# Kernel optimization log

Measured on AMD Instinct MI355X. Metric: run time of the kernel, lower is better.

## Reference

```python
import jax, jax.numpy as jnp
import numpy as np

NUM_FEAS = 4096
HID = 128
BATCH = 128


def setup_inputs() -> dict:
    key = jax.random.key(0)
    k1, k2, k3, k4 = jax.random.split(key, 4)
    batch_x = jax.random.normal(k1, (BATCH, NUM_FEAS), dtype=jnp.float32)
    C = jax.random.normal(k2, (1, HID), dtype=jnp.float32)
    W = jax.random.normal(k3, (NUM_FEAS, HID), dtype=jnp.float32)
    B = jax.random.normal(k4, (NUM_FEAS,), dtype=jnp.float32)
    return {"batch_x": batch_x, "C": C, "W": W, "B": B}


def reference(batch_x, C, W, B):
    # binarize input (matches (x > 0).float())
    x = (batch_x > 0).astype(jnp.float32)  # [B, F]
    # prefix sums: S_excl[b, i] = sum_{j < i} x[b, j] * W[j]   -> [B, F, H]
    contrib = x[:, :, None] * W[None, :, :]
    S = jnp.cumsum(contrib, axis=1)
    S_excl = jnp.concatenate([jnp.zeros_like(S[:, :1]), S[:, :-1]], axis=1)
    # hidden state for i >= 1: h_i = sigmoid(S_excl_i + C)
    h = jax.nn.sigmoid(S_excl + C[None, :, :])  # [B, F, H]
    # faithful quirk: for i == 0 the original uses raw C (no sigmoid)
    h = h.at[:, 0, :].set(jnp.broadcast_to(C[0], (x.shape[0], HID)))
    # logits z_i = h_i . W_i + B_i ; p_i = sigmoid(z_i)
    z = jnp.einsum('bfh,fh->bf', h, W) + B[None, :]
    # BCE(sum over features), stable via log_sigmoid
    log_p = jax.nn.log_sigmoid(z)
    log_q = jax.nn.log_sigmoid(-z)
    loss_per_sample = -jnp.sum(x * log_p + (1.0 - x) * log_q, axis=1)
    return jnp.mean(loss_per_sample)
```

## Files before the change

### kernel.cpp

```cpp
#include <hip/hip_runtime.h>

#define NFEAS 4096
#define HID   128
#define BATCH 128
#define NSUB  64
#define NCH   16
#define KF    256
#define L2E   1.4426950408889634f
#define LN2   0.6931471805599453f

__device__ __forceinline__ float scan64(float v) {
  float r = v; int y;
  y = __builtin_amdgcn_update_dpp(0, __float_as_int(r), 0x111, 0xF, 0xF, true); r += __int_as_float(y);
  y = __builtin_amdgcn_update_dpp(0, __float_as_int(r), 0x112, 0xF, 0xF, true); r += __int_as_float(y);
  y = __builtin_amdgcn_update_dpp(0, __float_as_int(r), 0x114, 0xF, 0xF, true); r += __int_as_float(y);
  y = __builtin_amdgcn_update_dpp(0, __float_as_int(r), 0x118, 0xF, 0xF, true); r += __int_as_float(y);
  y = __builtin_amdgcn_update_dpp(0, __float_as_int(r), 0x142, 0xA, 0xF, true); r += __int_as_float(y);
  y = __builtin_amdgcn_update_dpp(0, __float_as_int(r), 0x143, 0xC, 0xF, true); r += __int_as_float(y);
  return r;
}

__device__ __forceinline__ void scan64_x8(float& a, float& b, float& c, float& d,
                                          float& e, float& f, float& g, float& h) {
  int t0, t1, t2, t3, t4, t5, t6, t7;
#define S8(ctrl, rm)                                                              \
  t0 = __builtin_amdgcn_update_dpp(0, __float_as_int(a), ctrl, rm, 0xF, true);    \
  t1 = __builtin_amdgcn_update_dpp(0, __float_as_int(b), ctrl, rm, 0xF, true);    \
  t2 = __builtin_amdgcn_update_dpp(0, __float_as_int(c), ctrl, rm, 0xF, true);    \
  t3 = __builtin_amdgcn_update_dpp(0, __float_as_int(d), ctrl, rm, 0xF, true);    \
  t4 = __builtin_amdgcn_update_dpp(0, __float_as_int(e), ctrl, rm, 0xF, true);    \
  t5 = __builtin_amdgcn_update_dpp(0, __float_as_int(f), ctrl, rm, 0xF, true);    \
  t6 = __builtin_amdgcn_update_dpp(0, __float_as_int(g), ctrl, rm, 0xF, true);    \
  t7 = __builtin_amdgcn_update_dpp(0, __float_as_int(h), ctrl, rm, 0xF, true);    \
  a += __int_as_float(t0); b += __int_as_float(t1);                               \
  c += __int_as_float(t2); d += __int_as_float(t3);                               \
  e += __int_as_float(t4); f += __int_as_float(t5);                               \
  g += __int_as_float(t6); h += __int_as_float(t7);
  S8(0x111, 0xF) S8(0x112, 0xF) S8(0x114, 0xF) S8(0x118, 0xF)
  S8(0x142, 0xA) S8(0x143, 0xC)
#undef S8
}

__global__ __launch_bounds__(128) void chunk_sums_kernel(
    const float* __restrict__ x, const float* __restrict__ W,
    float* __restrict__ T)
{
  __shared__ float xm[64][8];
  const int c = blockIdx.x, g = blockIdx.y, t = threadIdx.x;

  {
    const int s = t >> 4, fb = (t & 15) << 2;
    const float4 v = *reinterpret_cast<const float4*>(
        &x[(size_t)(g * 8 + s) * NFEAS + c * 64 + fb]);
    xm[fb + 0][s] = v.x > 0.f ? 1.f : 0.f;
    xm[fb + 1][s] = v.y > 0.f ? 1.f : 0.f;
    xm[fb + 2][s] = v.z > 0.f ? 1.f : 0.f;
    xm[fb + 3][s] = v.w > 0.f ? 1.f : 0.f;
  }
  __syncthreads();

  float acc[8];
  #pragma unroll
  for (int s = 0; s < 8; ++s) acc[s] = 0.f;

  #pragma unroll 4
  for (int f = 0; f < 64; ++f) {
    const float wv = W[(size_t)(c * 64 + f) * HID + t];
    const float4 ma = *reinterpret_cast<const float4*>(&xm[f][0]);
    const float4 mb = *reinterpret_cast<const float4*>(&xm[f][4]);
    acc[0] = __builtin_fmaf(ma.x, wv, acc[0]);
    acc[1] = __builtin_fmaf(ma.y, wv, acc[1]);
    acc[2] = __builtin_fmaf(ma.z, wv, acc[2]);
    acc[3] = __builtin_fmaf(ma.w, wv, acc[3]);
    acc[4] = __builtin_fmaf(mb.x, wv, acc[4]);
    acc[5] = __builtin_fmaf(mb.y, wv, acc[5]);
    acc[6] = __builtin_fmaf(mb.z, wv, acc[6]);
    acc[7] = __builtin_fmaf(mb.w, wv, acc[7]);
  }
  #pragma unroll
  for (int s = 0; s < 8; ++s)
    T[((size_t)(g * 8 + s) * HID + t) * NSUB + c] = acc[s];
}

__global__ __launch_bounds__(256) void prefix_s2m_kernel(
    const float* __restrict__ T, const float* __restrict__ Cv,
    float* __restrict__ s2m)
{
  const int gw = blockIdx.x * 4 + (threadIdx.x >> 6);
  const int lane = threadIdx.x & 63;
  const int h = gw & 127;
  const float v = T[(size_t)gw * NSUB + lane];
  const float r = scan64(v);
  if ((lane & 3) == 0) {
    const float excl = r - v;
    s2m[(size_t)(lane >> 2) * (BATCH * HID) + gw] = -L2E * (excl + Cv[h]);
  }
}

__global__ __launch_bounds__(512, 4) void zpart_kernel(
    const float* __restrict__ x,   const float* __restrict__ W,
    const float* __restrict__ Cv,  const float* __restrict__ s2m,
    float* __restrict__ zpart)
{
  __shared__ float wt[32 * 256];
  __shared__ float s2l[16 * 32];
  __shared__ float cvl[32];

  const int c  = blockIdx.x;
  const int hq = blockIdx.y;
  const int bg = blockIdx.z;
  const int tid = threadIdx.x, lane = tid & 63, w = tid >> 6;
  const int base = c * KF;

  {
    const int hb = tid & 7, f0 = tid >> 3;
    const float* wp = W + (size_t)(base + f0) * HID + (hq << 5) + (hb << 2);
    const int colw = f0 ^ ((hb & 3) << 3);
    #pragma unroll
    for (int k = 0; k < 4; ++k) {
      const float4 v = *reinterpret_cast<const float4*>(wp + (size_t)(k << 6) * HID);
      float* q = &wt[((hb << 2) << 8) + colw + (k << 6)];
      q[0] = v.x; q[256] = v.y; q[512] = v.z; q[768] = v.w;
    }
  }
  {
    s2l[tid] = s2m[(size_t)c * (BATCH * HID) +
                   (size_t)(bg * 16 + (tid >> 5)) * HID + (hq << 5) + (tid & 31)];
  }
  if (tid < 32) cvl[tid] = Cv[(hq << 5) + tid];
  __syncthreads();

  const int sA = bg * 16 + w;
  const int sB = sA + 8;
  const float4 xvA = *reinterpret_cast<const float4*>(
      x + (size_t)sA * NFEAS + base + (lane << 2));
  const float4 xvB = *reinterpret_cast<const float4*>(
      x + (size_t)sB * NFEAS + base + (lane << 2));
  const float xA0 = xvA.x > 0.f ? 1.f : 0.f;
  const float xA1 = xvA.y > 0.f ? 1.f : 0.f;
  const float xA2 = xvA.z > 0.f ? 1.f : 0.f;
  const float xA3 = xvA.w > 0.f ? 1.f : 0.f;
  const float xB0 = xvB.x > 0.f ? 1.f : 0.f;
  const float xB1 = xvB.y > 0.f ? 1.f : 0.f;
  const float xB2 = xvB.z > 0.f ? 1.f : 0.f;
  const float xB3 = xvB.w > 0.f ? 1.f : 0.f;
  const bool qk = (c == 0) && (lane == 0);

  float zA0 = 0.f, zA1 = 0.f, zA2 = 0.f, zA3 = 0.f;
  float zB0 = 0.f, zB1 = 0.f, zB2 = 0.f, zB3 = 0.f;

  const float* s2A = &s2l[(w << 5)];
  const float* s2B = &s2l[((w + 8) << 5)];

  #pragma unroll
  for (int cg = 0; cg < 8; ++cg) {
    const int colx = (lane << 2) ^ ((cg & 3) << 3);
    const int rb = (cg << 2) * 256 + colx;
    const float4 wv0 = *reinterpret_cast<const float4*>(&wt[rb]);
    const float4 wv1 = *reinterpret_cast<const float4*>(&wt[rb + 256]);
    const float4 wv2 = *reinterpret_cast<const float4*>(&wt[rb + 512]);
    const float4 wv3 = *reinterpret_cast<const float4*>(&wt[rb + 768]);

#define PREP(P, wvJ, J)                                                        \
    const float P##m##J##0 = wvJ.x * P##0;                                     \
    const float P##m##J##1 = wvJ.y * P##1;                                     \
    const float P##m##J##2 = wvJ.z * P##2;                                     \
    float P##r##J = (P##m##J##0 + P##m##J##1) +                                \
                    (P##m##J##2 + wvJ.w * P##3);
    PREP(xA, wv0, 0) PREP(xA, wv1, 1) PREP(xA, wv2, 2) PREP(xA, wv3, 3)
    PREP(xB, wv0, 0) PREP(xB, wv1, 1) PREP(xB, wv2, 2) PREP(xB, wv3, 3)
#undef PREP
    const float pA0 = xAr0, pA1 = xAr1, pA2 = xAr2, pA3 = xAr3;
    const float pB0 = xBr0, pB1 = xBr1, pB2 = xBr2, pB3 = xBr3;

    scan64_x8(xAr0, xAr1, xAr2, xAr3, xBr0, xBr1, xBr2, xBr3);

#define FIN(P, S2, ZP0, ZP1, ZP2, ZP3, wvJ, rJ, psJ, J)                         \
    {                                                                           \
      const float smv = S2[(cg << 2) + J];                                      \
      const float e0 = rJ - psJ;                                                \
      const float e1 = e0 + P##m##J##0;                                         \
      const float e2 = e1 + P##m##J##1;                                         \
      const float e3 = e2 + P##m##J##2;                                         \
      float g0 = __builtin_amdgcn_rcpf(1.f + __builtin_amdgcn_exp2f(__builtin_fmaf(e0, -L2E, smv))); \
      const float g1 = __builtin_amdgcn_rcpf(1.f + __builtin_amdgcn_exp2f(__builtin_fmaf(e1, -L2E, smv))); \
      const float g2 = __builtin_amdgcn_rcpf(1.f + __builtin_amdgcn_exp2f(__builtin_fmaf(e2, -L2E, smv))); \
      const float g3 = __builtin_amdgcn_rcpf(1.f + __builtin_amdgcn_exp2f(__builtin_fmaf(e3, -L2E, smv))); \
      if (qk) g0 = cvl[(cg << 2) + J];           \
      ZP0 = __builtin_fmaf(g0, wvJ.x, ZP0);                                     \
      ZP1 = __builtin_fmaf(g1, wvJ.y, ZP1);                                     \
      ZP2 = __builtin_fmaf(g2, wvJ.z, ZP2);                                     \
      ZP3 = __builtin_fmaf(g3, wvJ.w, ZP3);                                     \
    }
    FIN(xA, s2A, zA0, zA1, zA2, zA3, wv0, xAr0, pA0, 0)
    FIN(xA, s2A, zA0, zA1, zA2, zA3, wv1, xAr1, pA1, 1)
    FIN(xA, s2A, zA0, zA1, zA2, zA3, wv2, xAr2, pA2, 2)
    FIN(xA, s2A, zA0, zA1, zA2, zA3, wv3, xAr3, pA3, 3)
    FIN(xB, s2B, zB0, zB1, zB2, zB3, wv0, xBr0, pB0, 0)
    FIN(xB, s2B, zB0, zB1, zB2, zB3, wv1, xBr1, pB1, 1)
    FIN(xB, s2B, zB0, zB1, zB2, zB3, wv2, xBr2, pB2, 2)
    FIN(xB, s2B, zB0, zB1, zB2, zB3, wv3, xBr3, pB3, 3)
#undef FIN
  }

  float4 za; za.x = zA0; za.y = zA1; za.z = zA2; za.w = zA3;
  float4 zb; zb.x = zB0; zb.y = zB1; zb.z = zB2; zb.w = zB3;
  *reinterpret_cast<float4*>(
      &zpart[((size_t)hq * BATCH + sA) * NFEAS + base + (lane << 2)]) = za;
  *reinterpret_cast<float4*>(
      &zpart[((size_t)hq * BATCH + sB) * NFEAS + base + (lane << 2)]) = zb;
}

__global__ __launch_bounds__(256) void bce_kernel(
    const float* __restrict__ x, const float* __restrict__ Bv,
    const float* __restrict__ zpart, float* __restrict__ lossb)
{
  __shared__ float sm[256];
  const int b = blockIdx.x, t = threadIdx.x;
  const size_t Q = (size_t)BATCH * NFEAS;
  float acc = 0.f;
  #pragma unroll
  for (int i = 0; i < NFEAS / 256; ++i) {
    const int f = i * 256 + t;
    const size_t o = (size_t)b * NFEAS + f;
    const float zt = ((zpart[o] + zpart[Q + o]) +
                      (zpart[2 * Q + o] + zpart[3 * Q + o])) + Bv[f];
    const float xf = x[o] > 0.f ? 1.f : 0.f;
    const float az = __builtin_fabsf(zt);
    const float ee = __builtin_amdgcn_exp2f(-L2E * az);
    acc += fmaxf(zt, 0.f) - xf * zt + LN2 * __builtin_amdgcn_logf(1.f + ee);
  }
  sm[t] = acc;
  __syncthreads();
  for (int s = 128; s > 0; s >>= 1) {
    if (t < s) sm[t] += sm[t + s];
    __syncthreads();
  }
  if (t == 0) lossb[b] = sm[0];
}

__global__ __launch_bounds__(128) void finalize_kernel(
    const float* __restrict__ lossb, float* __restrict__ out)
{
  __shared__ float sm[128];
  const int t = threadIdx.x;
  sm[t] = lossb[t];
  __syncthreads();
  for (int s = 64; s > 0; s >>= 1) {
    if (t < s) sm[t] += sm[t + s];
    __syncthreads();
  }
  if (t == 0) out[0] = sm[0] * (1.f / BATCH);
}

extern "C" void kernel_launch(void* const* d_in, const int* in_sizes, int n_in,
                              void* d_out, int out_size, void* d_ws, size_t ws_size,
                              hipStream_t stream)
{
  const float* x  = (const float*)d_in[0];
  const float* Cv = (const float*)d_in[1];
  const float* W  = (const float*)d_in[2];
  const float* Bv = (const float*)d_in[3];
  float* out = (float*)d_out;

  float* T     = (float*)d_ws;
  float* s2m   = T     + (size_t)BATCH * HID * NSUB;
  float* zpart = s2m   + (size_t)NCH * BATCH * HID;
  float* lossb = zpart + (size_t)4 * BATCH * NFEAS;

  chunk_sums_kernel<<<dim3(NSUB, BATCH / 8), 128, 0, stream>>>(x, W, T);
  prefix_s2m_kernel<<<dim3(BATCH * HID / 4), 256, 0, stream>>>(T, Cv, s2m);
  zpart_kernel<<<dim3(NCH, 4, BATCH / 16), 512, 0, stream>>>(x, W, Cv, s2m, zpart);
  bce_kernel<<<dim3(BATCH), 256, 0, stream>>>(x, Bv, zpart, lossb);
  finalize_kernel<<<1, 128, 0, stream>>>(lossb, out);
}
```

Before: 58.09 us.

## Fuse prefix scan into zpart kernel and widen BCE reduction grid

Removes the separate prefix_s2m kernel: each zpart block now sums the preceding chunk totals of T directly (a serial loop of up to 15 float4 loads per thread) to build its exclusive prefix in shared memory. The zpart grid order is changed so that blocks sharing W columns run adjacently, x loads are issued earlier, and outputs use nontemporal stores. The BCE kernel is spread over 512 blocks with float4 nontemporal loads, and finalize reduces 512 partials. This saves one launch and one intermediate round trip through memory, at the cost of redundant prefix summation in each zpart block.

```diff
diff --git a/kernel.cpp b/kernel.cpp
--- a/kernel.cpp
+++ b/kernel.cpp
@@ -9,16 +9,7 @@
 #define L2E   1.4426950408889634f
 #define LN2   0.6931471805599453f
 
-__device__ __forceinline__ float scan64(float v) {
-  float r = v; int y;
-  y = __builtin_amdgcn_update_dpp(0, __float_as_int(r), 0x111, 0xF, 0xF, true); r += __int_as_float(y);
-  y = __builtin_amdgcn_update_dpp(0, __float_as_int(r), 0x112, 0xF, 0xF, true); r += __int_as_float(y);
-  y = __builtin_amdgcn_update_dpp(0, __float_as_int(r), 0x114, 0xF, 0xF, true); r += __int_as_float(y);
-  y = __builtin_amdgcn_update_dpp(0, __float_as_int(r), 0x118, 0xF, 0xF, true); r += __int_as_float(y);
-  y = __builtin_amdgcn_update_dpp(0, __float_as_int(r), 0x142, 0xA, 0xF, true); r += __int_as_float(y);
-  y = __builtin_amdgcn_update_dpp(0, __float_as_int(r), 0x143, 0xC, 0xF, true); r += __int_as_float(y);
-  return r;
-}
+typedef float f32x4 __attribute__((ext_vector_type(4)));
 
 __device__ __forceinline__ void scan64_x8(float& a, float& b, float& c, float& d,
                                           float& e, float& f, float& g, float& h) {
@@ -82,35 +73,41 @@
     T[((size_t)(g * 8 + s) * HID + t) * NSUB + c] = acc[s];
 }
 
-__global__ __launch_bounds__(256) void prefix_s2m_kernel(
-    const float* __restrict__ T, const float* __restrict__ Cv,
-    float* __restrict__ s2m)
-{
-  const int gw = blockIdx.x * 4 + (threadIdx.x >> 6);
-  const int lane = threadIdx.x & 63;
-  const int h = gw & 127;
-  const float v = T[(size_t)gw * NSUB + lane];
-  const float r = scan64(v);
-  if ((lane & 3) == 0) {
-    const float excl = r - v;
-    s2m[(size_t)(lane >> 2) * (BATCH * HID) + gw] = -L2E * (excl + Cv[h]);
-  }
-}
-
 __global__ __launch_bounds__(512, 4) void zpart_kernel(
-    const float* __restrict__ x,   const float* __restrict__ W,
-    const float* __restrict__ Cv,  const float* __restrict__ s2m,
+    const float* __restrict__ x,  const float* __restrict__ W,
+    const float* __restrict__ Cv, const float* __restrict__ T,
     float* __restrict__ zpart)
 {
   __shared__ float wt[32 * 256];
   __shared__ float s2l[16 * 32];
   __shared__ float cvl[32];
 
-  const int c  = blockIdx.x;
-  const int hq = blockIdx.y;
-  const int bg = blockIdx.z;
+  const int bg = blockIdx.x;
+  const int c  = blockIdx.y;
+  const int hq = blockIdx.z;
   const int tid = threadIdx.x, lane = tid & 63, w = tid >> 6;
   const int base = c * KF;
+
+  const int sA = bg * 16 + w;
+  const int sB = sA + 8;
+  const float4 xvA = *reinterpret_cast<const float4*>(
+      x + (size_t)sA * NFEAS + base + (lane << 2));
+  const float4 xvB = *reinterpret_cast<const float4*>(
+      x + (size_t)sB * NFEAS + base + (lane << 2));
+
+  {
+    const int s = tid >> 5, ch = tid & 31;
+    const int b = bg * 16 + s, h = (hq << 5) + ch;
+    const float4* tr = reinterpret_cast<const float4*>(
+        T + ((size_t)b * HID + h) * NSUB);
+    float sum = 0.f;
+    for (int k = 0; k < c; ++k) {
+      const float4 v = tr[k];
+      sum += (v.x + v.y) + (v.z + v.w);
+    }
+    s2l[tid] = -L2E * (sum + Cv[h]);
+  }
+  if (tid < 32) cvl[tid] = Cv[(hq << 5) + tid];
 
   {
     const int hb = tid & 7, f0 = tid >> 3;
@@ -123,19 +120,8 @@
       q[0] = v.x; q[256] = v.y; q[512] = v.z; q[768] = v.w;
     }
   }
-  {
-    s2l[tid] = s2m[(size_t)c * (BATCH * HID) +
-                   (size_t)(bg * 16 + (tid >> 5)) * HID + (hq << 5) + (tid & 31)];
-  }
-  if (tid < 32) cvl[tid] = Cv[(hq << 5) + tid];
-  __syncthreads();
-
-  const int sA = bg * 16 + w;
-  const int sB = sA + 8;
-  const float4 xvA = *reinterpret_cast<const float4*>(
-      x + (size_t)sA * NFEAS + base + (lane << 2));
-  const float4 xvB = *reinterpret_cast<const float4*>(
-      x + (size_t)sB * NFEAS + base + (lane << 2));
+  __syncthreads();
+
   const float xA0 = xvA.x > 0.f ? 1.f : 0.f;
   const float xA1 = xvA.y > 0.f ? 1.f : 0.f;
   const float xA2 = xvA.z > 0.f ? 1.f : 0.f;
@@ -203,12 +189,12 @@
 #undef FIN
   }
 
-  float4 za; za.x = zA0; za.y = zA1; za.z = zA2; za.w = zA3;
-  float4 zb; zb.x = zB0; zb.y = zB1; zb.z = zB2; zb.w = zB3;
-  *reinterpret_cast<float4*>(
-      &zpart[((size_t)hq * BATCH + sA) * NFEAS + base + (lane << 2)]) = za;
-  *reinterpret_cast<float4*>(
-      &zpart[((size_t)hq * BATCH + sB) * NFEAS + base + (lane << 2)]) = zb;
+  f32x4 za; za.x = zA0; za.y = zA1; za.z = zA2; za.w = zA3;
+  f32x4 zb; zb.x = zB0; zb.y = zB1; zb.z = zB2; zb.w = zB3;
+  __builtin_nontemporal_store(za, reinterpret_cast<f32x4*>(
+      &zpart[((size_t)hq * BATCH + sA) * NFEAS + base + (lane << 2)]));
+  __builtin_nontemporal_store(zb, reinterpret_cast<f32x4*>(
+      &zpart[((size_t)hq * BATCH + sB) * NFEAS + base + (lane << 2)]));
 }
 
 __global__ __launch_bounds__(256) void bce_kernel(
@@ -216,37 +202,47 @@
     const float* __restrict__ zpart, float* __restrict__ lossb)
 {
   __shared__ float sm[256];
-  const int b = blockIdx.x, t = threadIdx.x;
+  const int b = blockIdx.x, q = blockIdx.y, t = threadIdx.x;
+  const int fb = (q << 10) + (t << 2);
   const size_t Q = (size_t)BATCH * NFEAS;
-  float acc = 0.f;
-  #pragma unroll
-  for (int i = 0; i < NFEAS / 256; ++i) {
-    const int f = i * 256 + t;
-    const size_t o = (size_t)b * NFEAS + f;
-    const float zt = ((zpart[o] + zpart[Q + o]) +
-                      (zpart[2 * Q + o] + zpart[3 * Q + o])) + Bv[f];
-    const float xf = x[o] > 0.f ? 1.f : 0.f;
-    const float az = __builtin_fabsf(zt);
-    const float ee = __builtin_amdgcn_exp2f(-L2E * az);
-    acc += fmaxf(zt, 0.f) - xf * zt + LN2 * __builtin_amdgcn_logf(1.f + ee);
-  }
-  sm[t] = acc;
+  const size_t o = (size_t)b * NFEAS + fb;
+
+  f32x4 zt = __builtin_nontemporal_load(
+      reinterpret_cast<const f32x4*>(&zpart[o]));
+  #pragma unroll
+  for (int s = 1; s < 4; ++s) {
+    const f32x4 v = __builtin_nontemporal_load(
+        reinterpret_cast<const f32x4*>(&zpart[(size_t)s * Q + o]));
+    zt.x += v.x; zt.y += v.y; zt.z += v.z; zt.w += v.w;
+  }
+  const float4 bv = *reinterpret_cast<const float4*>(Bv + fb);
+  zt.x += bv.x; zt.y += bv.y; zt.z += bv.z; zt.w += bv.w;
+  const float4 xv = *reinterpret_cast<const float4*>(&x[o]);
+
+#define BCE(zv, xvv)                                                      \
+  (fmaxf(zv, 0.f) - ((xvv) > 0.f ? (zv) : 0.f) +                          \
+   LN2 * __builtin_amdgcn_logf(1.f + __builtin_amdgcn_exp2f(-L2E * __builtin_fabsf(zv))))
+  const float li = (BCE(zt.x, xv.x) + BCE(zt.y, xv.y)) +
+                   (BCE(zt.z, xv.z) + BCE(zt.w, xv.w));
+#undef BCE
+
+  sm[t] = li;
   __syncthreads();
   for (int s = 128; s > 0; s >>= 1) {
     if (t < s) sm[t] += sm[t + s];
     __syncthreads();
   }
-  if (t == 0) lossb[b] = sm[0];
-}
-
-__global__ __launch_bounds__(128) void finalize_kernel(
+  if (t == 0) lossb[b * 4 + q] = sm[0];
+}
+
+__global__ __launch_bounds__(256) void finalize_kernel(
     const float* __restrict__ lossb, float* __restrict__ out)
 {
-  __shared__ float sm[128];
+  __shared__ float sm[256];
   const int t = threadIdx.x;
-  sm[t] = lossb[t];
-  __syncthreads();
-  for (int s = 64; s > 0; s >>= 1) {
+  sm[t] = lossb[t] + lossb[t + 256];
+  __syncthreads();
+  for (int s = 128; s > 0; s >>= 1) {
     if (t < s) sm[t] += sm[t + s];
     __syncthreads();
   }
@@ -264,13 +260,11 @@
   float* out = (float*)d_out;
 
   float* T     = (float*)d_ws;
-  float* s2m   = T     + (size_t)BATCH * HID * NSUB;
-  float* zpart = s2m   + (size_t)NCH * BATCH * HID;
+  float* zpart = T     + (size_t)BATCH * HID * NSUB;
   float* lossb = zpart + (size_t)4 * BATCH * NFEAS;
 
   chunk_sums_kernel<<<dim3(NSUB, BATCH / 8), 128, 0, stream>>>(x, W, T);
-  prefix_s2m_kernel<<<dim3(BATCH * HID / 4), 256, 0, stream>>>(T, Cv, s2m);
-  zpart_kernel<<<dim3(NCH, 4, BATCH / 16), 512, 0, stream>>>(x, W, Cv, s2m, zpart);
-  bce_kernel<<<dim3(BATCH), 256, 0, stream>>>(x, Bv, zpart, lossb);
-  finalize_kernel<<<1, 128, 0, stream>>>(lossb, out);
-}
+  zpart_kernel<<<dim3(BATCH / 16, NCH, 4), 512, 0, stream>>>(x, W, Cv, T, zpart);
+  bce_kernel<<<dim3(BATCH, 4), 256, 0, stream>>>(x, Bv, zpart, lossb);
+  finalize_kernel<<<1, 256, 0, stream>>>(lossb, out);
+}
```

Measured after the change: 57.46 us. No clear change (-1.1%).
